# Performance work log

Hardware: AMD Instinct MI355X
Metric: run time of the kernel (lower is better)

The kernel has to match this reference:

```python
import jax, jax.numpy as jnp
import numpy as np

V = 131072          # total vertices (hits) across all events
K = 64              # neighbours per vertex, col 0 == self
NSEG = 4            # number of events (row splits segments)
THRESHOLD = 0.5     # hierarchy score cut (layer's non-trainable threshold var)


def setup_inputs() -> dict:
    key = jax.random.key(0)
    k1, k2 = jax.random.split(key)
    score = jax.random.uniform(k1, (V, 1), dtype=jnp.float32)
    seg = V // NSEG
    base = (jnp.arange(V, dtype=jnp.int32) // seg) * seg
    # random neighbours constrained to the same segment; column 0 is self
    rnd = jax.random.randint(k2, (V, K - 1), 0, seg, dtype=jnp.int32) + base[:, None]
    nidxs = jnp.concatenate([jnp.arange(V, dtype=jnp.int32)[:, None], rnd], axis=1)
    row_splits = (jnp.arange(NSEG + 1, dtype=jnp.int32) * seg)
    return {"score": score, "nidxs": nidxs, "row_splits": row_splits}


def _local_group(score1, nidxs, row_splits, thr):
    """Greedy threshold-based neighbour grouping (HGCalML LocalGroup op).

    Vertices are visited per segment in descending score order. An unused
    vertex becomes a group seed; if its score > thr it absorbs all of its
    not-yet-used neighbours. Returns fixed-shape (-1 padded) outputs so the
    whole thing is jit-compatible.
    """
    V_, K_ = nidxs.shape
    seg_id = jnp.searchsorted(row_splits, jnp.arange(V_, dtype=row_splits.dtype),
                              side='right') - 1
    # per-segment descending-score order == tf.argsort(DESC) per row split
    order = jnp.lexsort((-score1, seg_id)).astype(jnp.int32)
    kcols = jnp.arange(K_)

    def step(state, v):
        used, assign, dirn, sel, seed, count = state
        is_new = jnp.logical_not(used[v])                 # v not grouped yet -> seed
        expand = score1[v] > thr                          # absorb neighbours?
        cand = jnp.where(expand, nidxs[v],
                         jnp.where(kcols == 0, v, -1))    # else only self
        safe = jnp.clip(cand, 0, V_ - 1)
        valid = (cand >= 0) & jnp.logical_not(used[safe]) & is_new
        used = used.at[safe].set(used[safe] | valid)
        assign = assign.at[safe].set(jnp.where(valid, count, assign[safe]))
        dirn = dirn.at[v].set(jnp.where(valid, cand, -1))
        sel = sel.at[count].set(jnp.where(is_new, v, sel[count]))
        seed = seed.at[v].set(seed[v] | is_new)
        count = count + is_new.astype(jnp.int32)
        return (used, assign, dirn, sel, seed, count), None

    init = (jnp.zeros(V_, dtype=bool),                 # used
            jnp.full(V_, -1, jnp.int32),               # backgather: seed rank per vertex
            jnp.full((V_, K_), -1, jnp.int32),         # directed neighbour idxs
            jnp.full(V_, -1, jnp.int32),               # selected seed vertices, -1 padded
            jnp.zeros(V_, dtype=bool),                 # seed mask
            jnp.int32(0))
    (used, assign, dirn, sel, seed, count), _ = jax.lax.scan(step, init, order)
    cs0 = jnp.concatenate([jnp.zeros(1, jnp.int32),
                           jnp.cumsum(seed.astype(jnp.int32))])
    rs_new = cs0[row_splits]                           # new row splits over seeds
    return rs_new, dirn, sel[:, None], assign, count


def reference(score, nidxs, row_splits):
    # layer: score = clip(score, 0, 1); per-segment argsort; LocalGroup
    score1 = jnp.clip(score.reshape(-1), 0.0, 1.0)
    rs_new, dirnidx, sel, backgather, n_sel = _local_group(score1, nidxs,
                                                           row_splits, THRESHOLD)
    # return_backscatter=True -> back = [V, sel]; we return sel (padded) + n_sel
    # outputs: directed nidx (V,K), selection idxs (V,1 padded with -1),
    #          backgather (V,), new row splits, number selected
    return dirnidx, sel, backgather, rs_new, n_sel
```

## Files before the change

kernel.cpp:

```cpp
#include <hip/hip_runtime.h>
#include <stdint.h>

#define INFU 0xFFFFFFFFu
#define LCAP 32768
#define NC 128

__global__ void __launch_bounds__(256) k_hist(const float* score, unsigned* bcnt,
                                              unsigned* claim, int* sel, unsigned* segE,
                                              int V, int SEGN, int initClaim){
  int v = blockIdx.x*blockDim.x+threadIdx.x; if (v>=V) return;
  if (initClaim) claim[v]=INFU;
  sel[v]=-1;
  float s = score[v]; s = fminf(fmaxf(s,0.f),1.f);
  int seg = v / SEGN;
  bool ex = (s > 0.5f);
  unsigned long long act = __ballot(true);
  unsigned long long mex = __ballot(ex);
  int lane = threadIdx.x & 63;
  int seg0 = __shfl(seg, 0);
  bool uni = (act == ~0ull) && (__shfl(seg,63) == seg0);
  if (uni){
    if (lane==0 && mex) atomicAdd(&segE[seg0], (unsigned)__popcll(mex));
  } else {
    if (ex) atomicAdd(&segE[seg], 1u);
  }
  int b = (int)(s*(float)SEGN); if (b>=SEGN) b=SEGN-1; if (b<0) b=0;
  int bd = SEGN-1-b;
  atomicAdd(&bcnt[(size_t)seg*SEGN+bd], 1u);
}

__global__ void __launch_bounds__(1024) k_scan0(const unsigned* bcnt, unsigned* bbase,
                                                unsigned* bfill, int SEGN){
  int seg = blockIdx.x; int tid = threadIdx.x; int lane = tid&63, wv = tid>>6;
  __shared__ unsigned s_wc[1024];
  const size_t base = (size_t)seg*SEGN;
  const int NP = (SEGN+1023)>>10;
  for (int p=0;p<NP;p++){
    int i = p*1024 + tid;
    unsigned x = (i<SEGN)? bcnt[base+i] : 0u;
    unsigned incl = x;
    #pragma unroll
    for (int off=1;off<64;off<<=1){ unsigned t=__shfl_up(incl,(unsigned)off); if (lane>=off) incl+=t; }
    if (lane==63) s_wc[p*16+wv]=incl;
  }
  __syncthreads();
  if (wv==0){
    unsigned carry=0; int n=NP*16;
    for (int ch=0; ch*64<n; ch++){
      int idx=ch*64+lane;
      unsigned x=(idx<n)? s_wc[idx]:0u;
      unsigned incl=x;
      #pragma unroll
      for (int off=1;off<64;off<<=1){ unsigned t=__shfl_up(incl,(unsigned)off); if (lane>=off) incl+=t; }
      if (idx<n) s_wc[idx]=carry+incl-x;
      carry += __shfl(incl,63);
    }
  }
  __syncthreads();
  for (int p=0;p<NP;p++){
    int i = p*1024 + tid;
    if (i<SEGN){
      unsigned x = bcnt[base+i];
      unsigned incl = x;
      #pragma unroll
      for (int off=1;off<64;off<<=1){ unsigned t=__shfl_up(incl,(unsigned)off); if (lane>=off) incl+=t; }
      bbase[base+i] = s_wc[p*16+wv] + incl - x;
      bfill[base+i] = 0u;
    }
  }
}

__global__ void __launch_bounds__(1024) k_scan(const unsigned* in, const unsigned* claim,
                                               unsigned* outExcl, unsigned* segTotal,
                                               int SEGN, int mode){
  int seg = blockIdx.x; int tid = threadIdx.x; int lane = tid&63, wv = tid>>6;
  __shared__ unsigned wsum[16];
  const int CH = (SEGN+1023)>>10;
  int i0 = tid*CH, i1 = i0+CH; if (i1>SEGN) i1=SEGN;
  const size_t base = (size_t)seg*SEGN;
  unsigned sum=0;
  for (int i=i0;i<i1;i++){
    unsigned x = (mode==0)? in[base+i] : ((claim[base+i]==INFU)?1u:0u);
    sum+=x;
  }
  unsigned incl=sum;
  for (int off=1;off<64;off<<=1){ unsigned t=__shfl_up(incl,(unsigned)off); if (lane>=off) incl+=t; }
  if (lane==63) wsum[wv]=incl;
  __syncthreads();
  unsigned wbase=0,total=0;
  for (int w=0;w<16;w++){ unsigned s=wsum[w]; if (w<wv) wbase+=s; total+=s; }
  unsigned run = wbase + incl - sum;
  for (int i=i0;i<i1;i++){
    unsigned x = (mode==0)? in[base+i] : ((claim[base+i]==INFU)?1u:0u);
    outExcl[base+i]=run; run+=x;
  }
  if (tid==0 && segTotal) segTotal[seg]=total;
}

__global__ void __launch_bounds__(256) k_scatter(const float* score, const unsigned* bbase,
                                                 unsigned* bfill, unsigned long long* slot,
                                                 int V, int SEGN){
  int v = blockIdx.x*blockDim.x+threadIdx.x; if (v>=V) return;
  float s = score[v]; s=fminf(fmaxf(s,0.f),1.f);
  int b=(int)(s*(float)SEGN); if(b>=SEGN)b=SEGN-1; if(b<0)b=0;
  int bd=SEGN-1-b; int seg=v/SEGN;
  size_t bk = (size_t)seg*SEGN+bd;
  unsigned pos = bbase[bk] + atomicAdd(&bfill[bk],1u);
  unsigned kb = ~__float_as_uint(s);
  slot[(size_t)seg*SEGN+pos] = ((unsigned long long)kb<<32) | (unsigned)v;
}

__global__ void __launch_bounds__(256) k_bsortbuild(const unsigned* bcnt, const unsigned* bbase,
                                                    unsigned long long* slot,
                                                    int* ord, unsigned* rnkv,
                                                    int V, int SEGN){
  int t = blockIdx.x*blockDim.x+threadIdx.x; if (t>=V) return;
  unsigned n = bcnt[t];
  if (!n) return;
  int seg = t / SEGN;
  const size_t segbase = (size_t)seg*SEGN;
  unsigned base = bbase[t];
  unsigned long long* a = slot + segbase + base;
  for (unsigned i=1;i<n;i++){
    unsigned long long key=a[i]; int j=(int)i-1;
    while (j>=0 && a[j]>key){ a[j+1]=a[j]; j--; }
    a[j+1]=key;
  }
  for (unsigned i=0;i<n;i++){
    int v = (int)(unsigned)(a[i] & 0xFFFFFFFFull);
    ord[segbase + base + i] = v;
    rnkv[v] = base + i;
  }
}

__global__ void __launch_bounds__(256) k_pack4(const int* ord, const unsigned* rnkv, const int* nidxs,
                                               const unsigned* segE, unsigned short* nbr16,
                                               int V, int K, int SEGN){
  const int K4 = K>>2;
  long long q = (long long)blockIdx.x*256 + threadIdx.x;
  if (q >= (long long)V*K4) return;
  int gr = (int)(q / K4); int k4 = (int)(q - (long long)gr*K4);
  int seg = gr / SEGN, r = gr - seg*SEGN;
  if (r >= (int)segE[seg]) return;
  int v = ord[gr];
  const int4 nn = *(const int4*)(nidxs + (size_t)v*K + (size_t)k4*4);
  ushort4 o;
  o.x=(unsigned short)rnkv[nn.x]; o.y=(unsigned short)rnkv[nn.y];
  o.z=(unsigned short)rnkv[nn.z]; o.w=(unsigned short)rnkv[nn.w];
  *(ushort4*)(nbr16 + (size_t)gr*K + (size_t)k4*4) = o;
}
__global__ void __launch_bounds__(256) k_pack(const int* ord, const unsigned* rnkv, const int* nidxs,
                                              const unsigned* segE, unsigned short* nbr16,
                                              int V, int K, int SEGN){
  long long t = (long long)blockIdx.x*256 + threadIdx.x;
  if (t >= (long long)V*K) return;
  int gr = (int)(t / K); int k = (int)(t - (long long)gr*K);
  int seg = gr / SEGN, r = gr - seg*SEGN;
  if (r >= (int)segE[seg]) return;
  int v = ord[gr];
  int w = nidxs[(size_t)v*K + k];
  nbr16[t] = (unsigned short)rnkv[w];
}

__global__ void __launch_bounds__(1024) k_greedy(const unsigned short* nbr16, const int* ord,
                                                 const unsigned* segEp,
                                                 unsigned* claim, unsigned* srank,
                                                 unsigned* segTotal, unsigned* absorb,
                                                 int SEGN, int K){
  __shared__ unsigned s_cl[LCAP/2];
  __shared__ unsigned char s_pos[LCAP];
  __shared__ unsigned s_cand[NC];
  __shared__ unsigned long long s_McLo[NC];
  __shared__ unsigned long long s_McHi[NC];
  __shared__ unsigned long long s_anyLo, s_anyHi;
  __shared__ unsigned long long s_bm[16];
  __shared__ unsigned s_ws[16];
  __shared__ unsigned s_base;
  __shared__ unsigned s_wcur;
  __shared__ unsigned long long s_v0, s_v1;
  const int seg = blockIdx.x, tid = threadIdx.x, lane = tid&63, wv = tid>>6;
  unsigned* clg = claim + (size_t)seg*SEGN;
  const size_t segbase = (size_t)seg*SEGN;
  const int E = (int)segEp[seg];
  const int cap = (LCAP < SEGN) ? LCAP : SEGN;
  const int capw = (cap+1)>>1;
  for (int i=tid; i<capw; i+=1024) s_cl[i]=0xFFFFFFFFu;
  for (int i=tid; i<((cap+3)>>2); i+=1024) ((unsigned*)s_pos)[i]=0u;
  if (tid<NC) s_cand[tid]=INFU;
  const unsigned long long lt_mask = (lane==0) ? 0ull : ((~0ull) >> (64-lane));
  unsigned wcursor = 0;
  for (;;){
    __syncthreads();
    if (tid<NC){
      unsigned pc = s_cand[tid];
      if (pc!=INFU && pc<(unsigned)cap) s_pos[pc]=0;
      s_cand[tid]=INFU; s_McLo[tid]=0ull; s_McHi[tid]=0ull;
    }
    if (tid==NC)   s_anyLo=0ull;
    if (tid==NC+1) s_anyHi=0ull;
    int found = 0;
    for (;;){
      unsigned r = wcursor + (unsigned)(wv*64 + lane);
      bool undec=false;
      if (r<(unsigned)E){
        if (r<(unsigned)cap)
          undec = (((s_cl[r>>1]>>((r&1)*16))&0xFFFFu)==0xFFFFu);
        else
          undec = (__hip_atomic_load(&clg[r], __ATOMIC_RELAXED, __HIP_MEMORY_SCOPE_AGENT)==INFU);
      }
      unsigned long long m = __ballot(undec);
      if (lane==0) s_bm[wv]=m;
      __syncthreads();
      unsigned long long mb = (lane<16)? s_bm[lane] : 0ull;
      int pc16 = (int)__popcll(mb);
      int incl = pc16;
      #pragma unroll
      for (int off=1; off<16; off<<=1){ int t=__shfl_up(incl,off); if (lane>=off) incl+=t; }
      int total = __shfl(incl, 15);
      int below = __shfl(incl, wv) - __shfl(pc16, wv);
      int pos = found + below + (int)__popcll(m & lt_mask);
      if (undec && pos<NC){
        s_cand[pos]=r;
        if (r<(unsigned)cap) s_pos[r]=(unsigned char)(pos+1);
      }
      if (undec && pos==NC-1) s_wcur=r+1;
      bool filled = (found+total>=NC);
      bool winend = (wcursor + 1024 >= (unsigned)E);
      __syncthreads();
      if (filled){ wcursor = s_wcur; found=NC; break; }
      found += total;
      if (winend){ wcursor=(unsigned)E; break; }
      wcursor += 1024;
    }
    const int ncand = found;
    if (!ncand) break;
    unsigned rwq[8], cq[8];
    #pragma unroll
    for (int q=0;q<8;q++){
      int c=(wv<<3)|q;
      cq[q] = (c<ncand) ? s_cand[c] : INFU;
    }
    #pragma unroll
    for (int q=0;q<8;q++){
      rwq[q]=INFU;
      if (cq[q]!=INFU && lane<K)
        rwq[q] = (unsigned)nbr16[(segbase + cq[q])*K + lane];
    }
    const bool fastmap = (s_cand[ncand-1] < (unsigned)cap);
    #pragma unroll
    for (int q=0;q<8;q++){
      int c=(wv<<3)|q;
      if (cq[q]!=INFU){
        unsigned rw = rwq[q];
        int p = -1;
        if (fastmap){
          if (rw<(unsigned)cap){ p = (int)s_pos[rw] - 1; }
        } else {
          int pp=0;
          if (s_cand[pp+64]<=rw) pp+=64;
          if (s_cand[pp+32]<=rw) pp+=32;
          if (s_cand[pp+16]<=rw) pp+=16;
          if (s_cand[pp+8 ]<=rw) pp+=8;
          if (s_cand[pp+4 ]<=rw) pp+=4;
          if (s_cand[pp+2 ]<=rw) pp+=2;
          if (s_cand[pp+1 ]<=rw) pp+=1;
          if (pp<ncand && s_cand[pp]==rw) p=pp;
        }
        if (lane<K && p>c){
          if (p<64){ atomicOr(&s_McLo[c], 1ull<<p);      atomicOr(&s_anyLo, 1ull<<p); }
          else     { atomicOr(&s_McHi[c], 1ull<<(p-64)); atomicOr(&s_anyHi, 1ull<<(p-64)); }
        }
      }
    }
    __syncthreads();
    if (wv==0){
      const int n0 = (ncand<64)? ncand : 64;
      const int n1 = ncand - n0;
      const unsigned long long nmask0 = (n0==64)? ~0ull : ((1ull<<n0)-1ull);
      unsigned long long Mj0 = s_McLo[lane];
      unsigned long long any0 = s_anyLo & nmask0;
      unsigned long long valid0 = (~any0) & nmask0;
      unsigned long long rem = any0;
      while (rem){
        int i=__builtin_ctzll(rem); rem &= rem-1;
        bool pred = ((valid0>>lane)&1ull) && (lane<i) && ((Mj0>>i)&1ull);
        if (__ballot(pred)==0ull) valid0 |= (1ull<<i);
      }
      unsigned long long valid1 = 0ull;
      if (n1>0){
        const unsigned long long nmask1 = (n1==64)? ~0ull : ((1ull<<n1)-1ull);
        unsigned long long sp = ((valid0>>lane)&1ull) ? s_McHi[lane] : 0ull;
        #pragma unroll
        for (int off=32; off; off>>=1)
          sp |= (unsigned long long)__shfl_xor((long long)sp, off);
        unsigned long long Mj1 = s_McHi[64+lane];
        unsigned long long any1 = s_anyHi & nmask1;
        valid1 = (~(any1|sp)) & nmask1;
        unsigned long long rem1 = any1 & ~sp;
        while (rem1){
          int i=__builtin_ctzll(rem1); rem1 &= rem1-1;
          bool pred = ((valid1>>lane)&1ull) && (lane<i) && ((Mj1>>i)&1ull);
          if (__ballot(pred)==0ull) valid1 |= (1ull<<i);
        }
      }
      if (lane==0){ s_v0=valid0; s_v1=valid1; }
    }
    __syncthreads();
    const unsigned long long v0 = s_v0, v1 = s_v1;
    #pragma unroll
    for (int q=0;q<8;q++){
      int c=(wv<<3)|q;
      bool isv = (c<64) ? (((v0>>c)&1ull)!=0ull) : (((v1>>(c-64))&1ull)!=0ull);
      if (cq[q]!=INFU && isv){
        unsigned rw=rwq[q], cr=cq[q];
        if (rw>cr && rw!=INFU){
          if (rw<(unsigned)cap){
            unsigned idx=rw>>1, sh=(rw&1)*16;
            unsigned old=s_cl[idx];
            for(;;){
              unsigned curv=(old>>sh)&0xFFFFu;
              if (cr>=curv) break;
              unsigned neu=(old & ~(0xFFFFu<<sh)) | (cr<<sh);
              unsigned prev=atomicCAS(&s_cl[idx], old, neu);
              if (prev==old) break;
              old=prev;
            }
          } else {
            atomicMin(&clg[rw], cr);
          }
        }
      }
    }
  }
  __syncthreads();
  if (cap == SEGN){
    if (tid==0) s_base=0;
    __syncthreads();
    for (int p=0; p<cap; p+=1024){
      int i = p + tid;
      bool live = (i<cap);
      unsigned c16 = 0xFFFFu;
      if (live) c16 = (s_cl[i>>1]>>((i&1)*16))&0xFFFFu;
      bool isSeed = live && (c16==0xFFFFu);
      unsigned long long m = __ballot(isSeed);
      if (lane==0) s_ws[wv]=(unsigned)__popcll(m);
      __syncthreads();
      unsigned wbase=0, tot=0;
      for (int w2=0;w2<16;w2++){ unsigned t2=s_ws[w2]; if (w2<wv) wbase+=t2; tot+=t2; }
      unsigned ex = s_base + wbase + (unsigned)__popcll(m & lt_mask);
      if (live){
        srank[segbase + i] = ex;
        absorb[ord[segbase + i]] = isSeed ? (unsigned)i : (unsigned)c16;
      }
      __syncthreads();
      if (tid==0) s_base += tot;
    }
    __syncthreads();
    if (tid==0) segTotal[seg] = s_base;
  } else {
    for (int r=tid; r<cap; r+=1024){
      unsigned c=(s_cl[r>>1]>>((r&1)*16))&0xFFFFu;
      clg[r] = (c==0xFFFFu) ? INFU : c;
    }
  }
}

__global__ void __launch_bounds__(256) k_absorb(const unsigned* rnkv, const unsigned* claim,
                                                unsigned* absorb, int V, int SEGN){
  int v = blockIdx.x*blockDim.x+threadIdx.x; if (v>=V) return;
  int seg = v / SEGN;
  unsigned r = rnkv[v];
  unsigned c = claim[(size_t)seg*SEGN + r];
  absorb[v] = (c==INFU)? r : c;
}

__global__ void __launch_bounds__(256) k_dirnAll4(const int* nidxs, const unsigned* rnkv,
                                                  const unsigned* absorb, const float* score,
                                                  const unsigned* segTotal,
                                                  const unsigned* srank,
                                                  int* dirn, int* sel, int* backg,
                                                  int* rs, int* nsel,
                                                  int V, int K, int SEGN, int NSEG){
  const int K4 = K>>2;
  long long q = (long long)blockIdx.x*256 + threadIdx.x;
  if (q >= (long long)V*K4) return;
  int v = (int)(q / K4); int k4 = (int)(q - (long long)v*K4);
  int seg = v / SEGN;
  if (q <= (long long)NSEG){
    unsigned run=0;
    for (int s=0;s<(int)q;s++) run+=segTotal[s];
    rs[q]=(int)run;
    if ((int)q==NSEG) nsel[0]=(int)run;
  }
  unsigned r = rnkv[v];
  unsigned a_self = absorb[v];
  bool seed = (a_self == r);
  if (k4==0){
    unsigned segOff=0;
    for (int s=0;s<seg;s++) segOff+=segTotal[s];
    unsigned g = segOff + srank[(size_t)seg*SEGN + a_self];
    backg[v] = (int)g;
    if (seed) sel[g] = v;
  }
  int4 o = make_int4(-1,-1,-1,-1);
  if (seed){
    float s = score[v]; s=fminf(fmaxf(s,0.f),1.f);
    if (!(s > 0.5f)){
      if (k4==0) o.x = v;
    } else {
      const int4 nn = *(const int4*)(nidxs + (size_t)v*K + (size_t)k4*4);
      if (absorb[nn.x]==r) o.x=nn.x;
      if (absorb[nn.y]==r) o.y=nn.y;
      if (absorb[nn.z]==r) o.z=nn.z;
      if (absorb[nn.w]==r) o.w=nn.w;
    }
  }
  *(int4*)(dirn + (size_t)v*K + (size_t)k4*4) = o;
}
__global__ void __launch_bounds__(256) k_dirnAll(const int* nidxs, const unsigned* rnkv,
                                                 const unsigned* absorb, const float* score,
                                                 const unsigned* segTotal,
                                                 const unsigned* srank,
                                                 int* dirn, int* sel, int* backg,
                                                 int* rs, int* nsel,
                                                 int V, int K, int SEGN, int NSEG){
  long long t = (long long)blockIdx.x*blockDim.x + threadIdx.x;
  if (t >= (long long)V*K) return;
  int v = (int)(t / K); int j = (int)(t - (long long)v*K);
  int seg = v / SEGN;
  if (t <= (long long)NSEG){
    unsigned run=0;
    for (int s=0;s<(int)t;s++) run+=segTotal[s];
    rs[t]=(int)run;
    if ((int)t==NSEG) nsel[0]=(int)run;
  }
  unsigned r = rnkv[v];
  unsigned a_self = absorb[v];
  bool seed = (a_self == r);
  if (j==0){
    unsigned segOff=0;
    for (int s=0;s<seg;s++) segOff+=segTotal[s];
    unsigned g = segOff + srank[(size_t)seg*SEGN + a_self];
    backg[v] = (int)g;
    if (seed) sel[g] = v;
  }
  int out = -1;
  if (seed){
    float s = score[v]; s=fminf(fmaxf(s,0.f),1.f);
    if (!(s > 0.5f)){
      out = (j==0)? v : -1;
    } else {
      int w = nidxs[(size_t)v*K + j];
      out = (absorb[w] == r)? w : -1;
    }
  }
  dirn[t] = out;
}

extern "C" void kernel_launch(void* const* d_in, const int* in_sizes, int n_in,
                              void* d_out, int out_size, void* d_ws, size_t ws_size,
                              hipStream_t stream) {
  const float* score   = (const float*)d_in[0];
  const int*   nidxs   = (const int*)d_in[1];
  (void)d_in[2];

  const int V    = in_sizes[0];
  const int K    = in_sizes[1] / V;
  const int NSEG = in_sizes[2] - 1;
  const int SEGN = V / NSEG;

  char* w = (char*)d_ws;
  unsigned long long* slot = (unsigned long long*)w;  w += (size_t)V*8;
  unsigned* bcnt  = (unsigned*)w; w += (size_t)V*4;
  unsigned* segE  = (unsigned*)w; w += 64;
  unsigned* bfill = (unsigned*)w; w += (size_t)V*4;
  unsigned* bbase = (unsigned*)w; w += (size_t)V*4;
  int*      ord   = (int*)w;      w += (size_t)V*4;
  unsigned* rnkv  = (unsigned*)w; w += (size_t)V*4;
  unsigned* claim = (unsigned*)w; w += (size_t)V*4;
  unsigned* srank = (unsigned*)w; w += (size_t)V*4;
  unsigned* segTotal = (unsigned*)w; w += 64;
  unsigned* absorb = bcnt;

  int* out      = (int*)d_out;
  int* out_dirn = out;
  int* out_sel  = out + (size_t)V*K;
  int* out_bg   = out_sel + V;
  int* out_rs   = out_bg + V;
  int* out_nsel = out_rs + (NSEG+1);

  unsigned short* nbr16 = (unsigned short*)out_dirn;

  hipMemsetAsync(bcnt, 0x00, (size_t)V*4 + 64, stream);

  int nb256 = (V + 255)/256;
  long long totVK = (long long)V*K;
  int nbVK = (int)((totVK + 255)/256);
  const bool vec4 = (K>=4) && ((K&3)==0);
  int nbQ = (int)(((long long)V*(K>>2) + 255)/256);
  const int initClaim = (SEGN > LCAP) ? 1 : 0;

  k_hist<<<nb256, 256, 0, stream>>>(score, bcnt, claim, out_sel, segE, V, SEGN, initClaim);
  k_scan0<<<NSEG, 1024, 0, stream>>>(bcnt, bbase, bfill, SEGN);
  k_scatter<<<nb256, 256, 0, stream>>>(score, bbase, bfill, slot, V, SEGN);
  k_bsortbuild<<<nb256, 256, 0, stream>>>(bcnt, bbase, slot, ord, rnkv, V, SEGN);
  if (vec4) k_pack4<<<nbQ, 256, 0, stream>>>(ord, rnkv, nidxs, segE, nbr16, V, K, SEGN);
  else      k_pack <<<nbVK, 256, 0, stream>>>(ord, rnkv, nidxs, segE, nbr16, V, K, SEGN);
  k_greedy<<<NSEG, 1024, 0, stream>>>(nbr16, ord, segE, claim, srank, segTotal, absorb,
                                      SEGN, K);
  if (SEGN > LCAP){
    k_scan<<<NSEG, 1024, 0, stream>>>(nullptr, claim, srank, segTotal, SEGN, 1);
    k_absorb<<<nb256, 256, 0, stream>>>(rnkv, claim, absorb, V, SEGN);
  }
  if (vec4) k_dirnAll4<<<nbQ, 256, 0, stream>>>(nidxs, rnkv, absorb, score, segTotal, srank,
                                                out_dirn, out_sel, out_bg, out_rs, out_nsel,
                                                V, K, SEGN, NSEG);
  else      k_dirnAll<<<nbVK, 256, 0, stream>>>(nidxs, rnkv, absorb, score, segTotal, srank,
                                                out_dirn, out_sel, out_bg, out_rs, out_nsel,
                                                V, K, SEGN, NSEG);
}
```

Measured before the change: 317.4 us.

## Skip neighbour-rank pack kernel; gather ranks directly in greedy via LDS rank table

When a segment fits in LDS (SEGN <= LCAP, which holds here with SEGN = 32768), the separate pack pass that builds a rank-ordered 16-bit neighbour table is no longer launched. The greedy kernel instead loads each segment's rank table into shared memory and, per candidate, reads ord then the raw nidxs row and maps each neighbour to its rank through that table. The position map shrinks to POSCAP entries to make room in LDS. This removes a full V*K gather-and-write pass but adds a dependent ord->nidxs load chain inside the serial greedy loop, which runs on only four blocks.

```diff
diff --git a/kernel.cpp b/kernel.cpp
--- a/kernel.cpp
+++ b/kernel.cpp
@@ -3,6 +3,7 @@
 
 #define INFU 0xFFFFFFFFu
 #define LCAP 32768
+#define POSCAP 20480
 #define NC 128
 
 __global__ void __launch_bounds__(256) k_hist(const float* score, unsigned* bcnt,
@@ -162,13 +163,15 @@
   nbr16[t] = (unsigned short)rnkv[w];
 }
 
-__global__ void __launch_bounds__(1024) k_greedy(const unsigned short* nbr16, const int* ord,
+__global__ void __launch_bounds__(1024) k_greedy(const unsigned short* nbr16, const int* nidxs,
+                                                 const int* ord, const unsigned* rnkv,
                                                  const unsigned* segEp,
                                                  unsigned* claim, unsigned* srank,
                                                  unsigned* segTotal, unsigned* absorb,
                                                  int SEGN, int K){
   __shared__ unsigned s_cl[LCAP/2];
-  __shared__ unsigned char s_pos[LCAP];
+  __shared__ unsigned short s_rnk[LCAP];
+  __shared__ unsigned char s_pos[POSCAP];
   __shared__ unsigned s_cand[NC];
   __shared__ unsigned long long s_McLo[NC];
   __shared__ unsigned long long s_McHi[NC];
@@ -183,17 +186,22 @@
   const size_t segbase = (size_t)seg*SEGN;
   const int E = (int)segEp[seg];
   const int cap = (LCAP < SEGN) ? LCAP : SEGN;
+  const bool useDirect = (cap == SEGN);
   const int capw = (cap+1)>>1;
   for (int i=tid; i<capw; i+=1024) s_cl[i]=0xFFFFFFFFu;
-  for (int i=tid; i<((cap+3)>>2); i+=1024) ((unsigned*)s_pos)[i]=0u;
+  for (int i=tid; i<((POSCAP+3)>>2); i+=1024) ((unsigned*)s_pos)[i]=0u;
+  if (useDirect){
+    for (int i=tid; i<SEGN; i+=1024) s_rnk[i] = (unsigned short)rnkv[segbase + i];
+  }
   if (tid<NC) s_cand[tid]=INFU;
   const unsigned long long lt_mask = (lane==0) ? 0ull : ((~0ull) >> (64-lane));
+  const int li = (lane<K)? lane : 0;
   unsigned wcursor = 0;
   for (;;){
     __syncthreads();
     if (tid<NC){
       unsigned pc = s_cand[tid];
-      if (pc!=INFU && pc<(unsigned)cap) s_pos[pc]=0;
+      if (pc!=INFU && pc<(unsigned)POSCAP) s_pos[pc]=0;
       s_cand[tid]=INFU; s_McLo[tid]=0ull; s_McHi[tid]=0ull;
     }
     if (tid==NC)   s_anyLo=0ull;
@@ -221,7 +229,7 @@
       int pos = found + below + (int)__popcll(m & lt_mask);
       if (undec && pos<NC){
         s_cand[pos]=r;
-        if (r<(unsigned)cap) s_pos[r]=(unsigned char)(pos+1);
+        if (r<(unsigned)POSCAP) s_pos[r]=(unsigned char)(pos+1);
       }
       if (undec && pos==NC-1) s_wcur=r+1;
       bool filled = (found+total>=NC);
@@ -240,13 +248,31 @@
       int c=(wv<<3)|q;
       cq[q] = (c<ncand) ? s_cand[c] : INFU;
     }
-    #pragma unroll
-    for (int q=0;q<8;q++){
-      rwq[q]=INFU;
-      if (cq[q]!=INFU && lane<K)
-        rwq[q] = (unsigned)nbr16[(segbase + cq[q])*K + lane];
-    }
-    const bool fastmap = (s_cand[ncand-1] < (unsigned)cap);
+    if (useDirect){
+      int vq[8], nq[8];
+      #pragma unroll
+      for (int q=0;q<8;q++){
+        unsigned cc = (cq[q]!=INFU)? cq[q] : 0u;
+        vq[q] = ord[segbase + cc];
+      }
+      #pragma unroll
+      for (int q=0;q<8;q++)
+        nq[q] = nidxs[(size_t)vq[q]*K + li];
+      #pragma unroll
+      for (int q=0;q<8;q++){
+        unsigned lv = (unsigned)(nq[q] - (int)segbase);
+        unsigned rr = s_rnk[lv];
+        rwq[q] = (cq[q]!=INFU && lane<K) ? rr : INFU;
+      }
+    } else {
+      #pragma unroll
+      for (int q=0;q<8;q++){
+        rwq[q]=INFU;
+        if (cq[q]!=INFU && lane<K)
+          rwq[q] = (unsigned)nbr16[(segbase + cq[q])*K + lane];
+      }
+    }
+    const bool fastmap = (s_cand[ncand-1] < (unsigned)POSCAP);
     #pragma unroll
     for (int q=0;q<8;q++){
       int c=(wv<<3)|q;
@@ -254,7 +280,7 @@
         unsigned rw = rwq[q];
         int p = -1;
         if (fastmap){
-          if (rw<(unsigned)cap){ p = (int)s_pos[rw] - 1; }
+          if (rw<(unsigned)POSCAP){ p = (int)s_pos[rw] - 1; }
         } else {
           int pp=0;
           if (s_cand[pp+64]<=rw) pp+=64;
@@ -504,10 +530,12 @@
   k_scan0<<<NSEG, 1024, 0, stream>>>(bcnt, bbase, bfill, SEGN);
   k_scatter<<<nb256, 256, 0, stream>>>(score, bbase, bfill, slot, V, SEGN);
   k_bsortbuild<<<nb256, 256, 0, stream>>>(bcnt, bbase, slot, ord, rnkv, V, SEGN);
-  if (vec4) k_pack4<<<nbQ, 256, 0, stream>>>(ord, rnkv, nidxs, segE, nbr16, V, K, SEGN);
-  else      k_pack <<<nbVK, 256, 0, stream>>>(ord, rnkv, nidxs, segE, nbr16, V, K, SEGN);
-  k_greedy<<<NSEG, 1024, 0, stream>>>(nbr16, ord, segE, claim, srank, segTotal, absorb,
-                                      SEGN, K);
+  if (SEGN > LCAP){
+    if (vec4) k_pack4<<<nbQ, 256, 0, stream>>>(ord, rnkv, nidxs, segE, nbr16, V, K, SEGN);
+    else      k_pack <<<nbVK, 256, 0, stream>>>(ord, rnkv, nidxs, segE, nbr16, V, K, SEGN);
+  }
+  k_greedy<<<NSEG, 1024, 0, stream>>>(nbr16, nidxs, ord, rnkv, segE, claim, srank, segTotal,
+                                      absorb, SEGN, K);
   if (SEGN > LCAP){
     k_scan<<<NSEG, 1024, 0, stream>>>(nullptr, claim, srank, segTotal, SEGN, 1);
     k_absorb<<<nb256, 256, 0, stream>>>(rnkv, claim, absorb, V, SEGN);
```

Measured after the change: 317.7 us, median of 2. No clear change (+0.1%).
